# Optimization experiments

Measured on AMD Instinct MI355X. Metric: run time of the kernel, lower is better.

Reference implementation:

```python
import jax, jax.numpy as jnp
import numpy as np

POOL = 7  # pool_size = (7, 7)


def setup_inputs() -> dict:
    key = jax.random.key(0)
    k1, k2, k3 = jax.random.split(key, 3)
    H = W = 64
    C = 128
    N = 10000  # hardcoded num_rois in the original layer
    feature_map = jax.random.normal(k1, (1, H, W, C), dtype=jnp.float32)
    # ROIs: [x1, y1, x2, y2] integer pixel coords with x2 > x1, y2 > y1
    xy1 = jax.random.randint(k2, (1, N, 2), 0, H // 2)
    size = jax.random.randint(k3, (1, N, 2), 4, H // 2)
    rois = jnp.concatenate([xy1, xy1 + size], axis=-1).astype(jnp.int32)
    # a few all-zero ROIs to exercise the zeros branch of the original layer
    rois = rois.at[0, :16].set(0)
    return {"feature_map": feature_map, "rois": rois}


def _roi_resize(fm, roi):
    """Crop fm[(y1:y2, x1:x2)] and bilinear-resize to (POOL, POOL).

    Matches tf.image.resize (bilinear, half-pixel centers, no antialias)
    applied to the integer-sliced crop. fm: (H, W, C), roi: (4,) int32.
    """
    rx1, ry1, rx2, ry2 = roi[0], roi[1], roi[2], roi[3]
    hh = jnp.maximum(ry2 - ry1, 1)
    ww = jnp.maximum(rx2 - rx1, 1)
    hf = hh.astype(jnp.float32)
    wf = ww.astype(jnp.float32)
    j = jnp.arange(POOL, dtype=jnp.float32)
    # half-pixel-center source coordinates within the crop, clamped
    yc = jnp.clip((j + 0.5) * hf / POOL - 0.5, 0.0, hf - 1.0)
    xc = jnp.clip((j + 0.5) * wf / POOL - 0.5, 0.0, wf - 1.0)
    y0 = jnp.floor(yc).astype(jnp.int32)
    x0 = jnp.floor(xc).astype(jnp.int32)
    y1i = jnp.minimum(y0 + 1, hh - 1)
    x1i = jnp.minimum(x0 + 1, ww - 1)
    wy = (yc - y0.astype(jnp.float32))[:, None, None]  # (P,1,1)
    wx = (xc - x0.astype(jnp.float32))[None, :, None]  # (1,P,1)
    # absolute indices into the full feature map
    ya0, ya1 = y0 + ry1, y1i + ry1
    xa0, xa1 = x0 + rx1, x1i + rx1
    r0 = fm[ya0]  # (P, W, C)
    r1 = fm[ya1]
    g00, g01 = r0[:, xa0], r0[:, xa1]  # (P, P, C)
    g10, g11 = r1[:, xa0], r1[:, xa1]
    top = g00 + wx * (g01 - g00)
    bot = g10 + wx * (g11 - g10)
    out = top + wy * (bot - top)
    # all-zero ROI -> zeros (original's special case)
    return jnp.where(jnp.all(roi == 0), jnp.zeros_like(out), out)


def reference(feature_map, rois):
    fm = feature_map[0]                      # (H, W, C)
    r = rois[0].astype(jnp.int32)            # (N, 4)
    pooled = jax.vmap(lambda roi: _roi_resize(fm, roi))(r)  # (N, P, P, C)
    n = r.shape[0]
    return pooled.reshape(1, n, POOL, POOL, -1)
```

## Files before the change

### kernel.cpp

```cpp
#include <hip/hip_runtime.h>


#define POOL 7
#define CH   128
#define FH   64
#define FW   64

__device__ __forceinline__ float4 lerp4(float4 a, float4 b, float w) {
    float4 r;
    r.x = fmaf(w, b.x - a.x, a.x);
    r.y = fmaf(w, b.y - a.y, a.y);
    r.z = fmaf(w, b.z - a.z, a.z);
    r.w = fmaf(w, b.w - a.w, a.w);
    return r;
}

__global__ __launch_bounds__(256) void roi_pool_kernel(
    const float* __restrict__ fm, const int* __restrict__ rois,
    float* __restrict__ out, int n_rois)
{
    const int n = blockIdx.x;
    if (n >= n_rois) return;

    const int rx1 = rois[n * 4 + 0];
    const int ry1 = rois[n * 4 + 1];
    const int rx2 = rois[n * 4 + 2];
    const int ry2 = rois[n * 4 + 3];

    const int tid  = threadIdx.x;
    const int posg = tid >> 5;
    const int lane = tid & 31;
    const int c    = lane << 2;

    float4* outv = (float4*)(out + (size_t)n * (POOL * POOL * CH));

    if ((rx1 | ry1 | rx2 | ry2) == 0) {
        float4 z = make_float4(0.f, 0.f, 0.f, 0.f);
        for (int pos = posg; pos < POOL * POOL; pos += 8)
            outv[pos * 32 + lane] = z;
        return;
    }

    const int hh = max(ry2 - ry1, 1);
    const int ww = max(rx2 - rx1, 1);
    const float hf = (float)hh;
    const float wf = (float)ww;

    for (int pos = posg; pos < POOL * POOL; pos += 8) {
        const int py = pos / POOL;
        const int px = pos - py * POOL;

        float yc = ((float)py + 0.5f) * hf / 7.0f - 0.5f;
        yc = fminf(fmaxf(yc, 0.0f), hf - 1.0f);
        float xc = ((float)px + 0.5f) * wf / 7.0f - 0.5f;
        xc = fminf(fmaxf(xc, 0.0f), wf - 1.0f);

        const int y0 = (int)floorf(yc);
        const int x0 = (int)floorf(xc);
        const int y1 = min(y0 + 1, hh - 1);
        const int x1 = min(x0 + 1, ww - 1);
        const float wy = yc - (float)y0;
        const float wx = xc - (float)x0;

        const int ya0 = y0 + ry1, ya1 = y1 + ry1;
        const int xa0 = x0 + rx1, xa1 = x1 + rx1;

        const float4 g00 = *(const float4*)(fm + ((size_t)ya0 * FW + xa0) * CH + c);
        const float4 g01 = *(const float4*)(fm + ((size_t)ya0 * FW + xa1) * CH + c);
        const float4 g10 = *(const float4*)(fm + ((size_t)ya1 * FW + xa0) * CH + c);
        const float4 g11 = *(const float4*)(fm + ((size_t)ya1 * FW + xa1) * CH + c);

        const float4 top = lerp4(g00, g01, wx);
        const float4 bot = lerp4(g10, g11, wx);
        const float4 res = lerp4(top, bot, wy);

        outv[pos * 32 + lane] = res;
    }
}

extern "C" void kernel_launch(void* const* d_in, const int* in_sizes, int n_in,
                              void* d_out, int out_size, void* d_ws, size_t ws_size,
                              hipStream_t stream) {
    const float* fm   = (const float*)d_in[0];
    const int*   rois = (const int*)d_in[1];
    float*       out  = (float*)d_out;
    const int n_rois  = in_sizes[1] / 4;

    roi_pool_kernel<<<n_rois, 256, 0, stream>>>(fm, rois, out, n_rois);
}
```

Baseline: 248.7 us.

## Precompute bilinear tables in LDS and use nontemporal output stores

The first 49 threads compute the per-position source byte offsets and interpolation weights once into shared memory, and every warp then reads them instead of recomputing coordinates. Output writes switch to nontemporal stores so the large write-only result does not pollute the cache, and launch bounds request higher occupancy. The cost is an extra __syncthreads and some LDS per block. The kernel is dominated by the roughly 250MB output write, so the gain is likely limited to the store path.

```diff
diff --git a/kernel.cpp b/kernel.cpp
--- a/kernel.cpp
+++ b/kernel.cpp
@@ -5,6 +5,9 @@
 #define CH   128
 #define FH   64
 #define FW   64
+#define NPOS (POOL * POOL)
+
+typedef float f32x4 __attribute__((ext_vector_type(4)));
 
 __device__ __forceinline__ float4 lerp4(float4 a, float4 b, float w) {
     float4 r;
@@ -15,10 +18,13 @@
     return r;
 }
 
-__global__ __launch_bounds__(256) void roi_pool_kernel(
+__global__ __launch_bounds__(256, 8) void roi_pool_kernel(
     const float* __restrict__ fm, const int* __restrict__ rois,
     float* __restrict__ out, int n_rois)
 {
+    __shared__ int4   tabi[NPOS];
+    __shared__ float2 tabf[NPOS];
+
     const int n = blockIdx.x;
     if (n >= n_rois) return;
 
@@ -30,51 +36,61 @@
     const int tid  = threadIdx.x;
     const int posg = tid >> 5;
     const int lane = tid & 31;
-    const int c    = lane << 2;
 
-    float4* outv = (float4*)(out + (size_t)n * (POOL * POOL * CH));
+    float4* outv = (float4*)(out + (size_t)n * (NPOS * CH)) + lane;
 
     if ((rx1 | ry1 | rx2 | ry2) == 0) {
         float4 z = make_float4(0.f, 0.f, 0.f, 0.f);
-        for (int pos = posg; pos < POOL * POOL; pos += 8)
-            outv[pos * 32 + lane] = z;
+        for (int pos = posg; pos < NPOS; pos += 8)
+            __builtin_nontemporal_store(*(f32x4*)&z, (f32x4*)&outv[pos * 32]);
         return;
     }
 
     const int hh = max(ry2 - ry1, 1);
     const int ww = max(rx2 - rx1, 1);
-    const float hf = (float)hh;
-    const float wf = (float)ww;
 
-    for (int pos = posg; pos < POOL * POOL; pos += 8) {
-        const int py = pos / POOL;
-        const int px = pos - py * POOL;
-
+    if (tid < NPOS) {
+        const int py = tid / POOL;
+        const int px = tid - py * POOL;
+        const float hf = (float)hh;
+        const float wf = (float)ww;
         float yc = ((float)py + 0.5f) * hf / 7.0f - 0.5f;
         yc = fminf(fmaxf(yc, 0.0f), hf - 1.0f);
         float xc = ((float)px + 0.5f) * wf / 7.0f - 0.5f;
         xc = fminf(fmaxf(xc, 0.0f), wf - 1.0f);
-
         const int y0 = (int)floorf(yc);
         const int x0 = (int)floorf(xc);
         const int y1 = min(y0 + 1, hh - 1);
         const int x1 = min(x0 + 1, ww - 1);
-        const float wy = yc - (float)y0;
-        const float wx = xc - (float)x0;
+        tabi[tid] = make_int4((y0 + ry1) * (FW * CH * 4),
+                              (y1 + ry1) * (FW * CH * 4),
+                              (x0 + rx1) * (CH * 4),
+                              (x1 + rx1) * (CH * 4));
+        tabf[tid] = make_float2(yc - (float)y0, xc - (float)x0);
+    }
+    __syncthreads();
 
-        const int ya0 = y0 + ry1, ya1 = y1 + ry1;
-        const int xa0 = x0 + rx1, xa1 = x1 + rx1;
+    const unsigned cb = (unsigned)(lane << 4);
+    const char* fmb = (const char*)fm;
 
-        const float4 g00 = *(const float4*)(fm + ((size_t)ya0 * FW + xa0) * CH + c);
-        const float4 g01 = *(const float4*)(fm + ((size_t)ya0 * FW + xa1) * CH + c);
-        const float4 g10 = *(const float4*)(fm + ((size_t)ya1 * FW + xa0) * CH + c);
-        const float4 g11 = *(const float4*)(fm + ((size_t)ya1 * FW + xa1) * CH + c);
+    for (int pos = posg; pos < NPOS; pos += 8) {
+        const int4   e = tabi[pos];
+        const float2 w = tabf[pos];
+        const unsigned o00 = (unsigned)(e.x + e.z) + cb;
+        const unsigned o01 = (unsigned)(e.x + e.w) + cb;
+        const unsigned o10 = (unsigned)(e.y + e.z) + cb;
+        const unsigned o11 = (unsigned)(e.y + e.w) + cb;
 
-        const float4 top = lerp4(g00, g01, wx);
-        const float4 bot = lerp4(g10, g11, wx);
-        const float4 res = lerp4(top, bot, wy);
+        const float4 g00 = *(const float4*)(fmb + o00);
+        const float4 g01 = *(const float4*)(fmb + o01);
+        const float4 g10 = *(const float4*)(fmb + o10);
+        const float4 g11 = *(const float4*)(fmb + o11);
 
-        outv[pos * 32 + lane] = res;
+        const float4 top = lerp4(g00, g01, w.y);
+        const float4 bot = lerp4(g10, g11, w.y);
+        float4 res = lerp4(top, bot, w.x);
+
+        __builtin_nontemporal_store(*(f32x4*)&res, (f32x4*)&outv[pos * 32]);
     }
 }
 
```

Measured after the change: 253.3 us. Within noise of the previous version (+1.9%).
